# Kernel optimization log

Hardware: AMD Instinct MI355X
Metric: run time of the kernel (lower is better)

Reference implementation:

```python
import jax, jax.numpy as jnp
import numpy as np

B, N, DIM = 2, 2048, 2048
H, DK, DV = 16, 64, 128
DIM_INNER = (DK + DV) * H  # 3072
EPS = 1e-12  # matches F.normalize clamp_min eps


def l2norm(t):
    n = jnp.linalg.norm(t, axis=-1, keepdims=True)
    return t / jnp.maximum(n, EPS)


def tanh_norm(t):
    n = jnp.linalg.norm(t, axis=-1, keepdims=True)
    return jnp.tanh(n) * (t / jnp.maximum(n, EPS))


def setup_inputs() -> dict:
    key = jax.random.key(0)
    k1, k2, k3, k4 = jax.random.split(key, 4)
    tokens = jax.random.normal(k1, (B, N, DIM), dtype=jnp.float32)
    # Linear weights stored as [in, out] (y = x @ W)
    Wqg = jax.random.normal(k2, (DIM, DIM_INNER), dtype=jnp.float32) * (DIM ** -0.5)
    Wkv = jax.random.normal(k3, (DIM, DIM_INNER), dtype=jnp.float32) * (DIM ** -0.5)
    Wo = jax.random.normal(k4, (DV * H, DIM), dtype=jnp.float32) * ((DV * H) ** -0.5)
    # LearnedScale log_scales, init log(1.0) = 0
    ls_iaw = jnp.zeros((H,), dtype=jnp.float32)  # inverse_acceptance_width (bias=1.0)
    ls_hws = jnp.zeros((H,), dtype=jnp.float32)  # head_wise_scale (bias=0.0)
    return {"tokens": tokens, "Wqg": Wqg, "Wkv": Wkv, "Wo": Wo,
            "ls_iaw": ls_iaw, "ls_hws": ls_hws}


def _split_heads(t):
    # [b, n, h*d] -> [b, h, n, d]
    b, n, _ = t.shape
    return t.reshape(b, n, H, -1).transpose(0, 2, 1, 3)


def reference(tokens, Wqg, Wkv, Wo, ls_iaw, ls_hws):
    qg = _split_heads(tokens @ Wqg)   # [b, h, n, dk+dv]
    kv = _split_heads(tokens @ Wkv)
    queries, gates = qg[..., :DK], qg[..., DK:]
    keys, values = kv[..., :DK], kv[..., DK:]
    queries, keys, values = l2norm(queries), l2norm(keys), l2norm(values)

    sim = jnp.einsum('bhid,bhjd->bhij', queries, keys)
    # r = 1 / (exp(log_scales) + 1)  (LearnedScale bias=1.0)
    r = 1.0 / (jnp.exp(ls_iaw) + 1.0)[None, :, None, None]
    attn = jnp.square(jax.nn.relu(1.0 - r * (1.0 - sim)))
    # NOTE: original code applies causal mask to `sim` AFTER computing `attn`,
    # so the mask has no effect on the output -- replicated faithfully here.
    aggr = jnp.einsum('bhij,bhjd->bhid', attn, values)
    out = tanh_norm(aggr) * jnp.tanh(jax.nn.silu(gates))
    out = out * jnp.exp(ls_hws)[None, :, None, None]  # head_wise_scale, bias=0
    out = out.transpose(0, 2, 1, 3).reshape(tokens.shape[0], tokens.shape[1], H * DV)
    return out @ Wo
```

## Files before the change

kernel.cpp:

```cpp
#include <hip/hip_runtime.h>
#include <hip/hip_bf16.h>
#include <stdint.h>


typedef unsigned short u16;
typedef __bf16 bf16x8 __attribute__((ext_vector_type(8)));
typedef u16 u16x8 __attribute__((ext_vector_type(8)));
typedef float f32x4 __attribute__((ext_vector_type(4)));
typedef float f32x16 __attribute__((ext_vector_type(16)));
typedef int i32x4 __attribute__((ext_vector_type(4)));

#define DEVINL __device__ __forceinline__

DEVINL u16 f2bf(float f) {
  union { float f; uint32_t u; } v; v.f = f;
  uint32_t r = (v.u + 0x7FFFu + ((v.u >> 16) & 1u)) >> 16;
  return (u16)r;
}
DEVINL float bf2f(u16 x) {
  union { uint32_t u; float f; } v; v.u = ((uint32_t)x) << 16;
  return v.f;
}
DEVINL bf16x8 as_bf(u16x8 v) { return __builtin_bit_cast(bf16x8, v); }

typedef const __attribute__((address_space(1))) uint32_t* gptr_t;
typedef __attribute__((address_space(3))) uint32_t* lptr_t;
DEVINL void gload_lds16(const void* g, void* l) {
  __builtin_amdgcn_global_load_lds((gptr_t)g, (lptr_t)l, 16, 0, 0);
}

DEVINL f32x4 mfma16(u16x8 a, u16x8 b, f32x4 c) {
  return __builtin_amdgcn_mfma_f32_16x16x32_bf16(as_bf(a), as_bf(b), c, 0, 0, 0);
}
DEVINL f32x16 mfma32(u16x8 a, u16x8 b, f32x16 c) {
  return __builtin_amdgcn_mfma_f32_32x32x16_bf16(as_bf(a), as_bf(b), c, 0, 0, 0);
}

__global__ void k_cvt(const float* __restrict__ src, u16* __restrict__ dst, int n) {
  int i = (blockIdx.x * blockDim.x + threadIdx.x) * 4;
  int stride = gridDim.x * blockDim.x * 4;
  for (; i < n; i += stride) {
    float4 f = *(const float4*)(src + i);
    ushort4 o;
    o.x = f2bf(f.x); o.y = f2bf(f.y); o.z = f2bf(f.z); o.w = f2bf(f.w);
    *(ushort4*)(dst + i) = o;
  }
}

__global__ void k_cvtT(const float* __restrict__ src, u16* __restrict__ dst, int R, int C) {
  __shared__ float tile[32][33];
  int c0 = blockIdx.x * 32, r0 = blockIdx.y * 32;
  int tc = threadIdx.x & 31, tr = threadIdx.x >> 5;
#pragma unroll
  for (int i = 0; i < 4; i++) {
    int r = tr + i * 8;
    tile[r][tc] = src[(size_t)(r0 + r) * C + c0 + tc];
  }
  __syncthreads();
#pragma unroll
  for (int i = 0; i < 4; i++) {
    int r = tr + i * 8;
    dst[(size_t)(c0 + r) * R + r0 + tc] = f2bf(tile[tc][r]);
  }
}

template <int BM, int BN, int WM, int WN, int F32OUT>
__global__ __launch_bounds__(512, 1) void k_gemm3(const u16* __restrict__ A,
                                                  const u16* __restrict__ Bt,
                                                  void* __restrict__ Cout,
                                                  int M, int Nt, int K) {
  constexpr int MI = WM / 16, NI = WN / 16;
  constexpr int NA = BM / 128, NB = BN / 128;
  constexpr int ABUF = BM * 32, BBUF = BN * 32;
  extern __shared__ char smem[];
  u16* As = (u16*)smem;
  u16* Bs = (u16*)(smem + 3 * ABUF * 2);

  const int tid = threadIdx.x, lane = tid & 63, wid = tid >> 6;

  const int NBM = M / BM, NBN = Nt / BN;
  const int bid = blockIdx.x;
  const int xcd = bid & 7, idx = bid >> 3;
  const int m0 = (idx % NBM) * BM;
  const int n0 = (xcd * (NBN / 8) + idx / NBM) * BN;

  const int wm = (wid >> 2) * WM, wn = (wid & 3) * WN;
  const int fr = lane & 15, hi = lane >> 4, frow = hi * 4;
  const int gsw = (hi ^ ((fr >> 1) & 3)) << 3;

  f32x4 acc[MI][NI] = {};

  const int sgran = (((lane & 3) ^ ((lane >> 3) & 3))) << 3;
  const u16* gA0 = A + (size_t)(m0 + wid * 16 * NA + (lane >> 2)) * K + sgran;
  const u16* gB0 = Bt + (size_t)(n0 + wid * 16 * NB + (lane >> 2)) * K + sgran;
  const int adst = wid * 16 * NA * 32;
  const int bdst = wid * 16 * NB * 32;
  const size_t r16 = (size_t)16 * K;

#define STAGE(T, S)                                                                  \
  {                                                                                  \
    const int kt_ = (T) * 32;                                                        \
    _Pragma("unroll") for (int i = 0; i < NA; i++)                                   \
        gload_lds16(gA0 + (size_t)i * r16 + kt_, As + (S)*ABUF + adst + i * 512);    \
    _Pragma("unroll") for (int i = 0; i < NB; i++)                                   \
        gload_lds16(gB0 + (size_t)i * r16 + kt_, Bs + (S)*BBUF + bdst + i * 512);    \
  }

  STAGE(0, 0);
  STAGE(1, 1);

  const int NTI = K >> 5;
  int slot = 0;
  for (int t = 0; t < NTI; t++) {
    if (t < NTI - 1) {
      if constexpr (NA + NB == 5) asm volatile("s_waitcnt vmcnt(5)" ::: "memory");
      else asm volatile("s_waitcnt vmcnt(3)" ::: "memory");
    } else {
      asm volatile("s_waitcnt vmcnt(0)" ::: "memory");
    }
    asm volatile("s_waitcnt lgkmcnt(0)" ::: "memory");
    __builtin_amdgcn_s_barrier();
    asm volatile("" ::: "memory");

    if (t + 2 < NTI) {
      const int s2 = (slot + 2 >= 3) ? slot - 1 : slot + 2;
      STAGE(t + 2, s2);
    }

    const u16* Ab = As + slot * ABUF;
    const u16* Bb = Bs + slot * BBUF;
    u16x8 af[MI], bf[NI];
#pragma unroll
    for (int mi = 0; mi < MI; mi++)
      af[mi] = *(const u16x8*)(Ab + (wm + mi * 16 + fr) * 32 + gsw);
#pragma unroll
    for (int ni = 0; ni < NI; ni++)
      bf[ni] = *(const u16x8*)(Bb + (wn + ni * 16 + fr) * 32 + gsw);

    __builtin_amdgcn_s_setprio(1);
#pragma unroll
    for (int mi = 0; mi < MI; mi++)
#pragma unroll
      for (int ni = 0; ni < NI; ni++)
        acc[mi][ni] = mfma16(af[mi], bf[ni], acc[mi][ni]);
    __builtin_amdgcn_s_setprio(0);

    slot = (slot + 1 >= 3) ? 0 : slot + 1;
  }
#undef STAGE

#pragma unroll
  for (int mi = 0; mi < MI; mi++)
#pragma unroll
    for (int ni = 0; ni < NI; ni++)
#pragma unroll
      for (int j = 0; j < 4; j++) {
        const size_t row = m0 + wm + mi * 16 + frow + j;
        const size_t col = n0 + wn + ni * 16 + fr;
        if (F32OUT) ((float*)Cout)[row * Nt + col] = acc[mi][ni][j];
        else ((u16*)Cout)[row * Nt + col] = f2bf(acc[mi][ni][j]);
      }
}

__global__ __launch_bounds__(256, 4) void k_norm(const u16* __restrict__ qgkv,
                                                 u16* __restrict__ qn, u16* __restrict__ kn,
                                                 u16* __restrict__ vnT, u16* __restrict__ gact) {
  __shared__ u16 vt[128 * 64];
  const int tid = threadIdx.x, lane = tid & 63, wid = tid >> 6;
  const int hb = blockIdx.y;
  const int h = hb & 15, b = hb >> 4;
  const int n0 = blockIdx.x * 64;

  for (int s = 0; s < 16; s++) {
    const int nl = wid * 16 + s;
    const int n = n0 + nl;
    const size_t bn = (size_t)b * 2048 + n;
    const size_t baseq = bn * 6144 + (size_t)h * 192;
    const size_t basek = baseq + 3072;

    float q = bf2f(qgkv[baseq + lane]);
    float g0 = bf2f(qgkv[baseq + 64 + lane]);
    float g1 = bf2f(qgkv[baseq + 128 + lane]);
    float k = bf2f(qgkv[basek + lane]);
    float v0 = bf2f(qgkv[basek + 64 + lane]);
    float v1 = bf2f(qgkv[basek + 128 + lane]);

    float qs = q * q, ks = k * k, vs = v0 * v0 + v1 * v1;
#pragma unroll
    for (int m = 1; m < 64; m <<= 1) {
      qs += __shfl_xor(qs, m);
      ks += __shfl_xor(ks, m);
      vs += __shfl_xor(vs, m);
    }
    float rq = 1.f / fmaxf(sqrtf(qs), 1e-12f);
    float rk = 1.f / fmaxf(sqrtf(ks), 1e-12f);
    float rv = 1.f / fmaxf(sqrtf(vs), 1e-12f);

    qn[((size_t)hb * 2048 + n) * 64 + lane] = f2bf(q * rq);
    kn[((size_t)hb * 2048 + n) * 64 + lane] = f2bf(k * rk);
    float s0 = g0 / (1.f + __expf(-g0));
    float s1 = g1 / (1.f + __expf(-g1));
    gact[((size_t)hb * 2048 + n) * 128 + lane] = f2bf(tanhf(s0));
    gact[((size_t)hb * 2048 + n) * 128 + 64 + lane] = f2bf(tanhf(s1));

    const int d0 = lane, d1 = 64 + lane;
    vt[d0 * 64 + (nl ^ ((d0 & 15) << 2))] = f2bf(v0 * rv);
    vt[d1 * 64 + (nl ^ ((d1 & 15) << 2))] = f2bf(v1 * rv);
  }
  __syncthreads();

#pragma unroll
  for (int p = 0; p < 8; p++) {
    const int d = p * 16 + (tid >> 4);
    const int nq = (tid & 15) * 4;
    const int cb = nq ^ ((d & 15) << 2);
    const int nq2 = (nq & ~12) | ((nq & 4) << 1) | ((nq & 8) >> 1);
    ushort4 o;
    o.x = vt[d * 64 + cb + 0];
    o.y = vt[d * 64 + cb + 1];
    o.z = vt[d * 64 + cb + 2];
    o.w = vt[d * 64 + cb + 3];
    *(ushort4*)(vnT + ((size_t)hb * 128 + d) * 2048 + n0 + nq2) = o;
  }
}

__global__ __launch_bounds__(256, 2) void k_attn(const u16* __restrict__ qn,
                                                 const u16* __restrict__ kn,
                                                 const u16* __restrict__ vnT,
                                                 const u16* __restrict__ gact,
                                                 const float* __restrict__ ls_iaw,
                                                 const float* __restrict__ ls_hws,
                                                 u16* __restrict__ pre_out) {
  extern __shared__ char smem[];
  u16* KsB = (u16*)smem;
  u16* VsB = (u16*)(smem + 16384);
  u16* Os = (u16*)smem;

  const int tid = threadIdx.x, lane = tid & 63, wid = tid >> 6;
  const int bid = blockIdx.y * 16 + blockIdx.x;
  const int bh = (bid & 7) * 4 + ((bid >> 3) & 3);
  const int n0 = (bid >> 5) * 128;
  const int h = bh & 15;
  const int l31 = lane & 31, L = lane >> 5, rb = l31 & 7;
  const float r = 1.f / (__expf(ls_iaw[h]) + 1.f);
  const float c1 = 1.f - r;
  const float whs = __expf(ls_hws[h]);

  const int wq = wid * 32;
  const u16* qrow = qn + ((size_t)bh * 2048 + n0 + wq + l31) * 64;
  u16x8 qf[4];
#pragma unroll
  for (int c = 0; c < 4; c++) qf[c] = *(const u16x8*)(qrow + c * 16 + L * 8);

  f32x16 acc[4] = {};
  const u16* kbase = kn + (size_t)bh * 2048 * 64;
  const u16* vbase = vnT + (size_t)bh * 128 * 2048;

  int ks_goff[2];
#pragma unroll
  for (int i = 0; i < 2; i++) {
    int row = wid * 16 + i * 8 + (lane >> 3);
    ks_goff[i] = row * 64 + (((lane & 7) ^ (row & 7)) << 3);
  }
  int vs_goff[4];
#pragma unroll
  for (int i = 0; i < 4; i++) {
    int row = wid * 32 + i * 8 + (lane >> 3);
    vs_goff[i] = row * 2048 + (((lane & 7) ^ (row & 7)) << 3);
  }

  {
    u16* KsC = KsB + wid * 1024;
    u16* VsC = VsB + wid * 2048;
#pragma unroll
    for (int i = 0; i < 2; i++) gload_lds16(kbase + ks_goff[i], KsC + i * 512);
#pragma unroll
    for (int i = 0; i < 4; i++) gload_lds16(vbase + vs_goff[i], VsC + i * 512);
  }

  int cur = 0;
  for (int t = 0; t < 32; t++) {
    asm volatile("s_waitcnt vmcnt(0) lgkmcnt(0)" ::: "memory");
    __builtin_amdgcn_s_barrier();
    asm volatile("" ::: "memory");

    if (t < 31) {
      const int kv0 = (t + 1) * 64;
      u16* KsC2 = KsB + (cur ^ 1) * 4096 + wid * 1024;
      u16* VsC2 = VsB + (cur ^ 1) * 8192 + wid * 2048;
#pragma unroll
      for (int i = 0; i < 2; i++) gload_lds16(kbase + (size_t)kv0 * 64 + ks_goff[i], KsC2 + i * 512);
#pragma unroll
      for (int i = 0; i < 4; i++) gload_lds16(vbase + (size_t)vs_goff[i] + kv0, VsC2 + i * 512);
    }

    const u16* KsC = KsB + cur * 4096;
    const u16* VsC = VsB + cur * 8192;

    f32x16 sT0 = {}, sT1 = {};
    __builtin_amdgcn_s_setprio(1);
#pragma unroll
    for (int c = 0; c < 4; c++) {
      u16x8 kf0 = *(const u16x8*)(KsC + (0 + l31) * 64 + (((2 * c + L) ^ rb) << 3));
      u16x8 kf1 = *(const u16x8*)(KsC + (32 + l31) * 64 + (((2 * c + L) ^ rb) << 3));
      sT0 = mfma32(kf0, qf[c], sT0);
      sT1 = mfma32(kf1, qf[c], sT1);
    }
    __builtin_amdgcn_s_setprio(0);

    uint32_t w[2][4][2];
#pragma unroll
    for (int m = 0; m < 4; m++)
#pragma unroll
      for (int p = 0; p < 2; p++) {
        float a0 = fmaxf(0.f, fmaf(r, sT0[4 * m + 2 * p], c1));
        float a1 = fmaxf(0.f, fmaf(r, sT0[4 * m + 2 * p + 1], c1));
        float b0 = fmaxf(0.f, fmaf(r, sT1[4 * m + 2 * p], c1));
        float b1 = fmaxf(0.f, fmaf(r, sT1[4 * m + 2 * p + 1], c1));
        w[0][m][p] = (uint32_t)f2bf(a0 * a0) | ((uint32_t)f2bf(a1 * a1) << 16);
        w[1][m][p] = (uint32_t)f2bf(b0 * b0) | ((uint32_t)f2bf(b1 * b1) << 16);
      }

    __builtin_amdgcn_s_setprio(1);
#pragma unroll
    for (int kt = 0; kt < 2; kt++)
#pragma unroll
      for (int pair = 0; pair < 2; pair++) {
        i32x4 pw;
        pw[0] = (int)w[kt][2 * pair][0];
        pw[1] = (int)w[kt][2 * pair][1];
        pw[2] = (int)w[kt][2 * pair + 1][0];
        pw[3] = (int)w[kt][2 * pair + 1][1];
        u16x8 pf = __builtin_bit_cast(u16x8, pw);
        const int chunk = 4 * kt + 2 * pair + L;
#pragma unroll
        for (int dt = 0; dt < 4; dt++) {
          u16x8 vf = *(const u16x8*)(VsC + (dt * 32 + l31) * 64 + ((chunk ^ rb) << 3));
          acc[dt] = mfma32(vf, pf, acc[dt]);
        }
      }
    __builtin_amdgcn_s_setprio(0);
    cur ^= 1;
  }

  float ss = 0.f;
#pragma unroll
  for (int dt = 0; dt < 4; dt++)
#pragma unroll
    for (int e = 0; e < 16; e++) { float x = acc[dt][e]; ss += x * x; }
  ss += __shfl_xor(ss, 32);
  float nn = sqrtf(ss);
  float scale = tanhf(nn) / fmaxf(nn, 1e-12f) * whs;

  __syncthreads();

  const int q = wq + l31;
  const size_t grow = ((size_t)bh * 2048 + n0 + q) * 128;
#pragma unroll
  for (int dt = 0; dt < 4; dt++)
#pragma unroll
    for (int m = 0; m < 4; m++) {
      const int d = dt * 32 + 8 * m + 4 * L;
      ushort4 gv = *(const ushort4*)(gact + grow + d);
      ushort4 o;
      o.x = f2bf(acc[dt][4 * m + 0] * scale * bf2f(gv.x));
      o.y = f2bf(acc[dt][4 * m + 1] * scale * bf2f(gv.y));
      o.z = f2bf(acc[dt][4 * m + 2] * scale * bf2f(gv.z));
      o.w = f2bf(acc[dt][4 * m + 3] * scale * bf2f(gv.w));
      *(ushort4*)(Os + q * 132 + d) = o;
    }
  __syncthreads();

  const int orow = tid >> 1, oc0 = (tid & 1) * 64;
  const size_t obase = ((size_t)(bh >> 4) * 2048 + n0 + orow) * 2048 + (size_t)h * 128 + oc0;
#pragma unroll
  for (int j = 0; j < 16; j++) {
    ushort4 v = *(const ushort4*)(Os + orow * 132 + oc0 + 4 * j);
    *(ushort4*)(pre_out + obase + 4 * j) = v;
  }
}

extern "C" void kernel_launch(void* const* d_in, const int* in_sizes, int n_in,
                              void* d_out, int out_size, void* d_ws, size_t ws_size,
                              hipStream_t stream) {
  (void)in_sizes; (void)n_in; (void)out_size; (void)ws_size;
  const float* tokens = (const float*)d_in[0];
  const float* Wqg = (const float*)d_in[1];
  const float* Wkv = (const float*)d_in[2];
  const float* Wo = (const float*)d_in[3];
  const float* ls_iaw = (const float*)d_in[4];
  const float* ls_hws = (const float*)d_in[5];
  float* out = (float*)d_out;
  char* ws = (char*)d_ws;

  u16* WoT = (u16*)(ws + 0);
  char* regA = ws + 8388608;
  u16* tok_bf = (u16*)(regA);
  u16* WqgkvT = (u16*)(regA + 16777216);
  u16* qn = (u16*)(regA);
  u16* kn = (u16*)(regA + 8388608);
  u16* vnT = (u16*)(regA + 16777216);
  u16* gact = (u16*)(regA + 33554432);
  char* regB = ws + 58720256;
  u16* qgkv_raw = (u16*)(regB);
  u16* pre_out = (u16*)(regB);

  k_cvt<<<4096, 256, 0, stream>>>(tokens, tok_bf, 8388608);
  k_cvtT<<<dim3(96, 64), 256, 0, stream>>>(Wqg, WqgkvT, 2048, 3072);
  k_cvtT<<<dim3(96, 64), 256, 0, stream>>>(Wkv, WqgkvT + (size_t)3072 * 2048, 2048, 3072);
  k_cvtT<<<dim3(64, 64), 256, 0, stream>>>(Wo, WoT, 2048, 2048);

  k_gemm3<256, 384, 128, 96, 0><<<256, 512, 122880, stream>>>(tok_bf, WqgkvT, qgkv_raw, 4096, 6144, 2048);

  k_norm<<<dim3(32, 32), 256, 0, stream>>>(qgkv_raw, qn, kn, vnT, gact);

  k_attn<<<dim3(16, 32), 256, 49152, stream>>>(qn, kn, vnT, gact, ls_iaw, ls_hws, pre_out);

  k_gemm3<128, 256, 64, 64, 1><<<256, 512, 73728, stream>>>(pre_out, WoT, out, 4096, 2048, 2048);
}
```

Measured before the change: 312.5 us.

## Replace QKV projection GEMM with double-buffered quadrant-pipelined 128x384 kernel

```diff
diff --git a/kernel.cpp b/kernel.cpp
--- a/kernel.cpp
+++ b/kernel.cpp
@@ -62,6 +62,116 @@
     int r = tr + i * 8;
     dst[(size_t)(c0 + r) * R + r0 + tc] = f2bf(tile[tc][r]);
   }
+}
+
+template <int MH, int NH>
+DEVINL void kp_quad(const u16* __restrict__ Ab, const u16* __restrict__ Bb,
+                    f32x4 (&acc)[2][2][2][3], int mq32, int nq48,
+                    int fr, int hi, int rb7) {
+  u16x8 af[2][2], bf[3][2];
+#pragma unroll
+  for (int mi = 0; mi < 2; mi++)
+#pragma unroll
+    for (int kk = 0; kk < 2; kk++) {
+      const int row = MH * 64 + mq32 + mi * 16 + fr;
+      af[mi][kk] = *(const u16x8*)(Ab + row * 64 + (((kk * 4 + hi) ^ rb7) << 3));
+    }
+#pragma unroll
+  for (int ni = 0; ni < 3; ni++)
+#pragma unroll
+    for (int kk = 0; kk < 2; kk++) {
+      const int row = NH * 192 + nq48 + ni * 16 + fr;
+      bf[ni][kk] = *(const u16x8*)(Bb + row * 64 + (((kk * 4 + hi) ^ rb7) << 3));
+    }
+  __builtin_amdgcn_s_setprio(1);
+#pragma unroll
+  for (int kk = 0; kk < 2; kk++)
+#pragma unroll
+    for (int mi = 0; mi < 2; mi++)
+#pragma unroll
+      for (int ni = 0; ni < 3; ni++)
+        acc[MH][mi][NH][ni] = mfma16(af[mi][kk], bf[ni][kk], acc[MH][mi][NH][ni]);
+  __builtin_amdgcn_s_setprio(0);
+}
+
+__global__ __launch_bounds__(512, 1) void k_gemmP(const u16* __restrict__ A,
+                                                  const u16* __restrict__ Bt,
+                                                  u16* __restrict__ C,
+                                                  int Nt, int K) {
+  extern __shared__ char smem[];
+  u16* As = (u16*)smem;
+  u16* Bs = (u16*)(smem + 32768);
+  const int tid = threadIdx.x, lane = tid & 63, wid = tid >> 6;
+
+  const int bid = blockIdx.x;
+  const int xcd = bid & 7, idx = bid >> 3;
+  const int m0 = (idx & 31) * 128;
+  const int n0 = (xcd * 2 + (idx >> 5)) * 384;
+
+  const int mq32 = (wid >> 2) * 32, nq48 = (wid & 3) * 48;
+  const int fr = lane & 15, hi = lane >> 4, frow = hi * 4, rb7 = fr & 7;
+
+  f32x4 acc[2][2][2][3] = {};
+
+  const int schunk = ((lane & 7) ^ ((lane >> 3) & 7)) << 3;
+  const int srow = wid * 8 + (lane >> 3);
+  const u16* ga0 = A + (size_t)(m0 + srow) * K + schunk;
+  const u16* gb0 = Bt + (size_t)(n0 + srow) * K + schunk;
+  const size_t l64 = (size_t)64 * K;
+  const int dwave = wid * 512;
+
+#define SA(P, L, KT) gload_lds16(ga0 + (size_t)(L) * l64 + (KT), As + (P) * 8192 + (L) * 4096 + dwave)
+#define SB(P, L, KT) gload_lds16(gb0 + (size_t)(L) * l64 + (KT), Bs + (P) * 24576 + (L) * 4096 + dwave)
+
+  SA(0, 0, 0); SB(0, 0, 0); SB(0, 1, 0); SB(0, 2, 0);
+  SA(0, 1, 0); SB(0, 3, 0); SB(0, 4, 0); SB(0, 5, 0);
+
+  const int NTI = K >> 6;
+  for (int t = 0; t < NTI; t++) {
+    const int p = t & 1, pn = p ^ 1;
+    const int ktn = (t < NTI - 1 ? t + 1 : t) << 6;
+    const u16* Ab = As + p * 8192;
+    const u16* Bb = Bs + p * 24576;
+
+    asm volatile("s_waitcnt vmcnt(4)" ::: "memory");
+    __builtin_amdgcn_s_barrier();
+    asm volatile("" ::: "memory");
+    SA(pn, 0, ktn); SB(pn, 0, ktn);
+    kp_quad<0, 0>(Ab, Bb, acc, mq32, nq48, fr, hi, rb7);
+
+    asm volatile("s_waitcnt vmcnt(5)" ::: "memory");
+    __builtin_amdgcn_s_barrier();
+    asm volatile("" ::: "memory");
+    SB(pn, 1, ktn); SB(pn, 2, ktn);
+    kp_quad<1, 0>(Ab, Bb, acc, mq32, nq48, fr, hi, rb7);
+
+    asm volatile("s_waitcnt vmcnt(4)" ::: "memory");
+    __builtin_amdgcn_s_barrier();
+    asm volatile("" ::: "memory");
+    SA(pn, 1, ktn); SB(pn, 3, ktn);
+    kp_quad<0, 1>(Ab, Bb, acc, mq32, nq48, fr, hi, rb7);
+
+    SB(pn, 4, ktn); SB(pn, 5, ktn);
+    kp_quad<1, 1>(Ab, Bb, acc, mq32, nq48, fr, hi, rb7);
+  }
+#undef SA
+#undef SB
+  asm volatile("s_waitcnt vmcnt(0)" ::: "memory");
+
+#pragma unroll
+  for (int mh = 0; mh < 2; mh++)
+#pragma unroll
+    for (int mi = 0; mi < 2; mi++)
+#pragma unroll
+      for (int nh = 0; nh < 2; nh++)
+#pragma unroll
+        for (int ni = 0; ni < 3; ni++)
+#pragma unroll
+          for (int j = 0; j < 4; j++) {
+            const size_t row = m0 + mh * 64 + mq32 + mi * 16 + frow + j;
+            const size_t col = n0 + nh * 192 + nq48 + ni * 16 + fr;
+            C[row * Nt + col] = f2bf(acc[mh][mi][nh][ni][j]);
+          }
 }
 
 template <int BM, int BN, int WM, int WN, int F32OUT>
@@ -410,7 +520,7 @@
   k_cvtT<<<dim3(96, 64), 256, 0, stream>>>(Wkv, WqgkvT + (size_t)3072 * 2048, 2048, 3072);
   k_cvtT<<<dim3(64, 64), 256, 0, stream>>>(Wo, WoT, 2048, 2048);
 
-  k_gemm3<256, 384, 128, 96, 0><<<256, 512, 122880, stream>>>(tok_bf, WqgkvT, qgkv_raw, 4096, 6144, 2048);
+  k_gemmP<<<512, 512, 131072, stream>>>(tok_bf, WqgkvT, qgkv_raw, 6144, 2048);
 
   k_norm<<<dim3(32, 32), 256, 0, stream>>>(qgkv_raw, qn, kn, vnT, gact);
 
```

Measured after the change: 286.5 us. 8.3% less time.
